# Kernel optimization log

Hardware: AMD Instinct MI355X
Metric: run time of the kernel (lower is better)

Reference implementation:

```python
import jax, jax.numpy as jnp
import numpy as np

# NOTE: the original torch code writes `torch.tensor(10 ^ -18)` which is Python
# bitwise XOR, i.e. the constant -28 (NOT 1e-18). We replicate that exact math.
RULE_OFFSET = -28.0


def setup_inputs() -> dict:
    key = jax.random.key(0)
    k0, k1, k2, k3 = jax.random.split(key, 4)
    batch, n_rules, n_fea = 8192, 256, 128
    data = jax.random.normal(k0, (batch, n_fea), dtype=jnp.float32)
    para_mu = jax.random.uniform(k1, (n_rules, n_fea), dtype=jnp.float32)
    para_sigma = jax.random.uniform(k2, (n_rules, n_fea), dtype=jnp.float32)
    para_w3 = jax.random.uniform(k3, (n_rules, n_fea + 1), dtype=jnp.float32)
    return {"data": data, "para_mu": para_mu, "para_sigma": para_sigma, "para_w3": para_w3}


def reference(data, para_mu, para_sigma, para_w3):
    # Gaussian fuzzification exponents: (batch, n_rules, n_fea)
    diff = data[:, None, :] - para_mu[None, :, :]
    exponent = -(diff ** 2) / (2.0 * para_sigma ** 2)
    # prod over features of exp(.) == exp(sum over features) -- same math, fused.
    layer_rule = jnp.exp(jnp.sum(exponent, axis=2))  # (batch, n_rules)
    layer_rule = layer_rule + RULE_OFFSET
    inv_frn = 1.0 / jnp.sum(layer_rule, axis=1, keepdims=True)  # (batch, 1)
    layer_normalize = layer_rule * inv_frn  # (batch, n_rules)
    # TSK consequent: w3[:,0] + sum_f w3[:,1:] * x
    layer_conq = para_w3[:, 0][None, :] + jnp.einsum('bf,rf->br', data, para_w3[:, 1:])
    layer_out_tsk = jnp.sum(layer_normalize * layer_conq, axis=1)  # (batch,)
    return jax.nn.sigmoid(layer_out_tsk)
```

## Files before the change

### kernel.cpp

```cpp
#include <hip/hip_runtime.h>
#include <math.h>

#define NR 256
#define NF 128
#define BCOLS 32

typedef short  s16x8  __attribute__((ext_vector_type(8)));
typedef __bf16 bf16x8 __attribute__((ext_vector_type(8)));
typedef float  f32x16 __attribute__((ext_vector_type(16)));

__device__ __forceinline__ unsigned short f2bf(float x) {
    unsigned int u = __float_as_uint(x);
    unsigned int r = (u + 0x7FFFu + ((u >> 16) & 1u)) >> 16;
    return (unsigned short)r;
}
__device__ __forceinline__ float bf2f(unsigned short b) {
    return __uint_as_float(((unsigned int)b) << 16);
}
__device__ __forceinline__ bf16x8 as_bf(s16x8 v) {
    return __builtin_bit_cast(bf16x8, v);
}
__device__ __forceinline__ f32x16 mfma_bf16(s16x8 a, s16x8 b, f32x16 acc) {
    return __builtin_amdgcn_mfma_f32_32x32x16_bf16(as_bf(a), as_bf(b), acc, 0, 0, 0);
}

__global__ __launch_bounds__(256) void prep2_kernel(
    const float* __restrict__ mu, const float* __restrict__ sigma,
    const float* __restrict__ w3,
    unsigned short* __restrict__ PH, unsigned short* __restrict__ PL,
    unsigned short* __restrict__ WC,
    float* __restrict__ Cr, float* __restrict__ W0)
{
    const int blk = blockIdx.x;
    if (blk < 32) {
        const int t    = blk * 256 + threadIdx.x;
        const int e    = t >> 6;
        const int lane = t & 63;
        const int rt   = e >> 4;
        const int ks2  = e & 15;
        const bool second = (ks2 >= 8);
        const int fb   = (ks2 & 7) * 16 + (lane >> 5) * 8;
        const int rule = rt * 32 + (lane & 31);

        const float* mrow = mu    + (size_t)rule * NF + fb;
        const float* srow = sigma + (size_t)rule * NF + fb;
        const float* wrow = w3    + (size_t)rule * (NF + 1) + 1 + fb;

        s16x8 vh, vl, vw;
        #pragma unroll
        for (int j = 0; j < 8; ++j) {
            const float s  = srow[j];
            const float m  = mrow[j];
            const float w  = wrow[j];
            const float u2 = -0.5f / fmaxf(s * s, 1e-30f);
            const float val = second ? (-2.0f * u2 * m) : u2;
            const unsigned short hh = f2bf(val);
            vh[j] = (short)hh;
            vl[j] = (short)f2bf(val - bf2f(hh));
            const unsigned short wh = f2bf(w);
            vw[j] = (short)(second ? f2bf(w - bf2f(wh)) : wh);
        }
        ((s16x8*)PH)[t] = vh;
        ((s16x8*)PL)[t] = vl;
        ((s16x8*)WC)[t] = vw;
    } else {
        const int rg   = blk - 32;
        const int rl   = threadIdx.x >> 3;
        const int jj   = threadIdx.x & 7;
        const int rule = rg * 32 + rl;
        const float* mrow = mu    + (size_t)rule * NF + jj * 16;
        const float* srow = sigma + (size_t)rule * NF + jj * 16;
        float cc = 0.f;
        #pragma unroll
        for (int q = 0; q < 16; q += 4) {
            const float4 s4 = *(const float4*)(srow + q);
            const float4 m4 = *(const float4*)(mrow + q);
            cc += (-0.5f / fmaxf(s4.x * s4.x, 1e-30f)) * m4.x * m4.x;
            cc += (-0.5f / fmaxf(s4.y * s4.y, 1e-30f)) * m4.y * m4.y;
            cc += (-0.5f / fmaxf(s4.z * s4.z, 1e-30f)) * m4.z * m4.z;
            cc += (-0.5f / fmaxf(s4.w * s4.w, 1e-30f)) * m4.w * m4.w;
        }
        cc += __shfl_down(cc, 4);
        cc += __shfl_down(cc, 2);
        cc += __shfl_down(cc, 1);
        if (jj == 0) {
            Cr[rule] = cc;
            W0[rule] = w3[(size_t)rule * (NF + 1)];
        }
    }
}

__global__ __launch_bounds__(512) void fnn_mfma(
    const float* __restrict__ data,
    const unsigned short* __restrict__ PH, const unsigned short* __restrict__ PL,
    const unsigned short* __restrict__ WC,
    const float* __restrict__ Cr, const float* __restrict__ W0,
    float* __restrict__ out)
{
    __shared__ s16x8 sBH[16][64], sBL[16][64];
    __shared__ float sCr[NR], sW0[NR];
    __shared__ float redD[8][BCOLS], redN[8][BCOLS];

    const int tid = threadIdx.x;
    if (tid < NR) sCr[tid] = Cr[tid];
    else          sW0[tid - NR] = W0[tid - NR];

    const int b0 = blockIdx.x * BCOLS;

    {
        const int bks = tid >> 6;
        const int bln = tid & 63;
        const float* p = data + (size_t)(b0 + (bln & 31)) * NF
                              + bks * 16 + (bln >> 5) * 8;
        const float4 v0 = *(const float4*)(p);
        const float4 v1 = *(const float4*)(p + 4);
        const float dv[8] = {v0.x, v0.y, v0.z, v0.w, v1.x, v1.y, v1.z, v1.w};
        s16x8 e_d, e_dl, e_d2, e_d2l;
        #pragma unroll
        for (int j = 0; j < 8; ++j) {
            const float d  = dv[j];
            const float d2 = d * d;
            const unsigned short dh  = f2bf(d);
            const unsigned short d2h = f2bf(d2);
            e_d  [j] = (short)dh;
            e_dl [j] = (short)f2bf(d  - bf2f(dh));
            e_d2 [j] = (short)d2h;
            e_d2l[j] = (short)f2bf(d2 - bf2f(d2h));
        }
        sBH[bks    ][bln] = e_d2;
        sBL[bks    ][bln] = e_d2l;
        sBH[bks + 8][bln] = e_d;
        sBL[bks + 8][bln] = e_dl;
    }
    __syncthreads();

    const int wv   = tid >> 6;
    const int lane = tid & 63;
    const int col  = lane & 31;
    const int half = lane >> 5;

    const s16x8* PHp = (const s16x8*)PH + (size_t)wv * 16 * 64 + lane;
    const s16x8* PLp = (const s16x8*)PL + (size_t)wv * 16 * 64 + lane;
    const s16x8* WCp = (const s16x8*)WC + (size_t)wv * 16 * 64 + lane;

    f32x16 accS0, accS1, accQ;
    #pragma unroll
    for (int e = 0; e < 16; ++e) { accS0[e] = 0.f; accS1[e] = 0.f; accQ[e] = 0.f; }

    s16x8 a0 = PHp[0], a1 = PLp[0], a2 = WCp[0];
    #pragma unroll 1
    for (int ks = 0; ks < 16; ++ks) {
        const int nofs = ((ks < 15) ? (ks + 1) : ks) * 64;
        const s16x8 n0 = PHp[nofs];
        const s16x8 n1 = PLp[nofs];
        const s16x8 n2 = WCp[nofs];

        const s16x8 bh = sBH[ks][lane];
        const s16x8 bl = sBL[ks][lane];
        accS0 = mfma_bf16(a0, bh, accS0);
        accS1 = mfma_bf16(a1, bh, accS1);
        accS1 = mfma_bf16(a0, bl, accS1);
        if (ks < 8) {
            accQ = mfma_bf16(a2, sBH[ks + 8][lane], accQ);
            accQ = mfma_bf16(a2, sBL[ks + 8][lane], accQ);
        } else {
            accQ = mfma_bf16(a2, bh, accQ);
        }
        a0 = n0; a1 = n1; a2 = n2;
    }

    float den_p = 0.f, num_p = 0.f;
    #pragma unroll
    for (int reg = 0; reg < 16; ++reg) {
        const int rloc = (reg & 3) + 8 * (reg >> 2) + 4 * half;
        const int rule = wv * 32 + rloc;
        const float S  = accS0[reg] + accS1[reg] + sCr[rule];
        const float rv = __expf(fminf(S, 0.f)) - 28.0f;
        const float cq = accQ[reg] + sW0[rule];
        den_p += rv;
        num_p += rv * cq;
    }
    den_p += __shfl_xor(den_p, 32);
    num_p += __shfl_xor(num_p, 32);
    if (half == 0) { redD[wv][col] = den_p; redN[wv][col] = num_p; }
    __syncthreads();

    if (tid < BCOLS) {
        float den = 0.f, num = 0.f;
        #pragma unroll
        for (int w = 0; w < 8; ++w) { den += redD[w][tid]; num += redN[w][tid]; }
        out[b0 + tid] = 1.0f / (1.0f + __expf(-(num / den)));
    }
}

#define TBF 8
__global__ __launch_bounds__(256) void fnn_fused(
    const float* __restrict__ data,
    const float* __restrict__ mu, const float* __restrict__ sigma,
    const float* __restrict__ w3,
    float* __restrict__ out)
{
    __shared__ float d_tile[TBF][NF];
    __shared__ float red[TBF][2][4];

    const int tid = threadIdx.x;
    const int b0  = blockIdx.x * TBF;
    {
        const float4* src = (const float4*)(data + (size_t)b0 * NF);
        ((float4*)(&d_tile[0][0]))[tid] = src[tid];
    }
    __syncthreads();

    const float* mu_r = mu    + (size_t)tid * NF;
    const float* sg_r = sigma + (size_t)tid * NF;
    const float* w_r  = w3    + (size_t)tid * (NF + 1);

    float S[TBF], Q[TBF];
    #pragma unroll
    for (int b = 0; b < TBF; ++b) { S[b] = 0.f; Q[b] = 0.f; }

    #pragma unroll 2
    for (int f = 0; f < NF; f += 4) {
        const float4 m4 = *(const float4*)(mu_r + f);
        const float4 s4 = *(const float4*)(sg_r + f);
        const float w0 = w_r[1 + f + 0], w1 = w_r[1 + f + 1];
        const float w2 = w_r[1 + f + 2], w3v = w_r[1 + f + 3];
        float4 c4;
        c4.x = -0.5f / fmaxf(s4.x * s4.x, 1e-30f);
        c4.y = -0.5f / fmaxf(s4.y * s4.y, 1e-30f);
        c4.z = -0.5f / fmaxf(s4.z * s4.z, 1e-30f);
        c4.w = -0.5f / fmaxf(s4.w * s4.w, 1e-30f);
        #pragma unroll
        for (int b = 0; b < TBF; ++b) {
            const float4 d4 = *(const float4*)(&d_tile[b][f]);
            float t;
            t = d4.x - m4.x; S[b] = fmaf(t * t, c4.x, S[b]); Q[b] = fmaf(d4.x, w0,  Q[b]);
            t = d4.y - m4.y; S[b] = fmaf(t * t, c4.y, S[b]); Q[b] = fmaf(d4.y, w1,  Q[b]);
            t = d4.z - m4.z; S[b] = fmaf(t * t, c4.z, S[b]); Q[b] = fmaf(d4.z, w2,  Q[b]);
            t = d4.w - m4.w; S[b] = fmaf(t * t, c4.w, S[b]); Q[b] = fmaf(d4.w, w3v, Q[b]);
        }
    }

    const float bias = w_r[0];
    #pragma unroll
    for (int b = 0; b < TBF; ++b) {
        float rule = __expf(S[b]) - 28.0f;
        float rc   = rule * (bias + Q[b]);
        #pragma unroll
        for (int off = 32; off > 0; off >>= 1) {
            rule += __shfl_down(rule, off);
            rc   += __shfl_down(rc,   off);
        }
        if ((tid & 63) == 0) {
            red[b][0][tid >> 6] = rule;
            red[b][1][tid >> 6] = rc;
        }
    }
    __syncthreads();
    if (tid < TBF) {
        const float den = red[tid][0][0] + red[tid][0][1] + red[tid][0][2] + red[tid][0][3];
        const float num = red[tid][1][0] + red[tid][1][1] + red[tid][1][2] + red[tid][1][3];
        out[b0 + tid] = 1.0f / (1.0f + __expf(-(num / den)));
    }
}

extern "C" void kernel_launch(void* const* d_in, const int* in_sizes, int n_in,
                              void* d_out, int out_size, void* d_ws, size_t ws_size,
                              hipStream_t stream) {
    const float* data  = (const float*)d_in[0];
    const float* mu    = (const float*)d_in[1];
    const float* sigma = (const float*)d_in[2];
    const float* w3    = (const float*)d_in[3];
    float* out = (float*)d_out;

    const int batch = in_sizes[0] / NF;
    const size_t need = 3u * 65536u * sizeof(unsigned short) + 2u * NR * sizeof(float);

    if (ws_size >= need && (batch % BCOLS) == 0) {
        unsigned short* PH = (unsigned short*)d_ws;
        unsigned short* PL = PH + 65536;
        unsigned short* WC = PL + 65536;
        float* Cr = (float*)(WC + 65536);
        float* W0 = Cr + NR;
        prep2_kernel<<<40, 256, 0, stream>>>(mu, sigma, w3, PH, PL, WC, Cr, W0);
        fnn_mfma<<<batch / BCOLS, 512, 0, stream>>>(data, PH, PL, WC, Cr, W0, out);
    } else {
        fnn_fused<<<batch / TBF, 256, 0, stream>>>(data, mu, sigma, w3, out);
    }
}
```

Baseline: 18.26 us.

## Fuse parameter prep into main MFMA kernel and drop low-part corrections

Removes the separate prep kernel and workspace buffers. Each block now recomputes the per-rule constants and the bf16 A operands from mu, sigma and w3 on the fly. The lo-part MFMA corrections for the quadratic term are dropped, going from three accumulators to one and cutting MFMA count. This saves a kernel launch but repeats the parameter transform and division in every block (256 blocks), and the lower bf16 precision in the exponent sum risks accuracy.

Result: slower. 33.56 us (+83.7%).

```diff
diff --git a/kernel.cpp b/kernel.cpp
--- a/kernel.cpp
+++ b/kernel.cpp
@@ -3,7 +3,6 @@
 
 #define NR 256
 #define NF 128
-#define BCOLS 32
 
 typedef short  s16x8  __attribute__((ext_vector_type(8)));
 typedef __bf16 bf16x8 __attribute__((ext_vector_type(8)));
@@ -24,88 +23,18 @@
     return __builtin_amdgcn_mfma_f32_32x32x16_bf16(as_bf(a), as_bf(b), acc, 0, 0, 0);
 }
 
-__global__ __launch_bounds__(256) void prep2_kernel(
+__global__ __launch_bounds__(512) void fnn_one(
+    const float* __restrict__ data,
     const float* __restrict__ mu, const float* __restrict__ sigma,
     const float* __restrict__ w3,
-    unsigned short* __restrict__ PH, unsigned short* __restrict__ PL,
-    unsigned short* __restrict__ WC,
-    float* __restrict__ Cr, float* __restrict__ W0)
-{
-    const int blk = blockIdx.x;
-    if (blk < 32) {
-        const int t    = blk * 256 + threadIdx.x;
-        const int e    = t >> 6;
-        const int lane = t & 63;
-        const int rt   = e >> 4;
-        const int ks2  = e & 15;
-        const bool second = (ks2 >= 8);
-        const int fb   = (ks2 & 7) * 16 + (lane >> 5) * 8;
-        const int rule = rt * 32 + (lane & 31);
-
-        const float* mrow = mu    + (size_t)rule * NF + fb;
-        const float* srow = sigma + (size_t)rule * NF + fb;
-        const float* wrow = w3    + (size_t)rule * (NF + 1) + 1 + fb;
-
-        s16x8 vh, vl, vw;
-        #pragma unroll
-        for (int j = 0; j < 8; ++j) {
-            const float s  = srow[j];
-            const float m  = mrow[j];
-            const float w  = wrow[j];
-            const float u2 = -0.5f / fmaxf(s * s, 1e-30f);
-            const float val = second ? (-2.0f * u2 * m) : u2;
-            const unsigned short hh = f2bf(val);
-            vh[j] = (short)hh;
-            vl[j] = (short)f2bf(val - bf2f(hh));
-            const unsigned short wh = f2bf(w);
-            vw[j] = (short)(second ? f2bf(w - bf2f(wh)) : wh);
-        }
-        ((s16x8*)PH)[t] = vh;
-        ((s16x8*)PL)[t] = vl;
-        ((s16x8*)WC)[t] = vw;
-    } else {
-        const int rg   = blk - 32;
-        const int rl   = threadIdx.x >> 3;
-        const int jj   = threadIdx.x & 7;
-        const int rule = rg * 32 + rl;
-        const float* mrow = mu    + (size_t)rule * NF + jj * 16;
-        const float* srow = sigma + (size_t)rule * NF + jj * 16;
-        float cc = 0.f;
-        #pragma unroll
-        for (int q = 0; q < 16; q += 4) {
-            const float4 s4 = *(const float4*)(srow + q);
-            const float4 m4 = *(const float4*)(mrow + q);
-            cc += (-0.5f / fmaxf(s4.x * s4.x, 1e-30f)) * m4.x * m4.x;
-            cc += (-0.5f / fmaxf(s4.y * s4.y, 1e-30f)) * m4.y * m4.y;
-            cc += (-0.5f / fmaxf(s4.z * s4.z, 1e-30f)) * m4.z * m4.z;
-            cc += (-0.5f / fmaxf(s4.w * s4.w, 1e-30f)) * m4.w * m4.w;
-        }
-        cc += __shfl_down(cc, 4);
-        cc += __shfl_down(cc, 2);
-        cc += __shfl_down(cc, 1);
-        if (jj == 0) {
-            Cr[rule] = cc;
-            W0[rule] = w3[(size_t)rule * (NF + 1)];
-        }
-    }
-}
-
-__global__ __launch_bounds__(512) void fnn_mfma(
-    const float* __restrict__ data,
-    const unsigned short* __restrict__ PH, const unsigned short* __restrict__ PL,
-    const unsigned short* __restrict__ WC,
-    const float* __restrict__ Cr, const float* __restrict__ W0,
     float* __restrict__ out)
 {
     __shared__ s16x8 sBH[16][64], sBL[16][64];
     __shared__ float sCr[NR], sW0[NR];
-    __shared__ float redD[8][BCOLS], redN[8][BCOLS];
+    __shared__ float redD[8][32], redN[8][32];
 
     const int tid = threadIdx.x;
-    if (tid < NR) sCr[tid] = Cr[tid];
-    else          sW0[tid - NR] = W0[tid - NR];
-
-    const int b0 = blockIdx.x * BCOLS;
+    const int b0  = blockIdx.x * 32;
 
     {
         const int bks = tid >> 6;
@@ -132,6 +61,26 @@
         sBH[bks + 8][bln] = e_d;
         sBL[bks + 8][bln] = e_dl;
     }
+
+    {
+        const int r   = tid >> 1;
+        const int seg = tid & 1;
+        const float* mrow = mu    + (size_t)r * NF + seg * 64;
+        const float* srow = sigma + (size_t)r * NF + seg * 64;
+        float cc = 0.f;
+        #pragma unroll 4
+        for (int q = 0; q < 64; q += 4) {
+            const float4 s4 = *(const float4*)(srow + q);
+            const float4 m4 = *(const float4*)(mrow + q);
+            cc += (-0.5f / fmaxf(s4.x * s4.x, 1e-30f)) * m4.x * m4.x;
+            cc += (-0.5f / fmaxf(s4.y * s4.y, 1e-30f)) * m4.y * m4.y;
+            cc += (-0.5f / fmaxf(s4.z * s4.z, 1e-30f)) * m4.z * m4.z;
+            cc += (-0.5f / fmaxf(s4.w * s4.w, 1e-30f)) * m4.w * m4.w;
+        }
+        cc += __shfl_xor(cc, 1);
+        if (seg == 0) sCr[r] = cc;
+        if (tid < NR) sW0[tid] = w3[(size_t)tid * (NF + 1)];
+    }
     __syncthreads();
 
     const int wv   = tid >> 6;
@@ -139,34 +88,56 @@
     const int col  = lane & 31;
     const int half = lane >> 5;
 
-    const s16x8* PHp = (const s16x8*)PH + (size_t)wv * 16 * 64 + lane;
-    const s16x8* PLp = (const s16x8*)PL + (size_t)wv * 16 * 64 + lane;
-    const s16x8* WCp = (const s16x8*)WC + (size_t)wv * 16 * 64 + lane;
-
-    f32x16 accS0, accS1, accQ;
-    #pragma unroll
-    for (int e = 0; e < 16; ++e) { accS0[e] = 0.f; accS1[e] = 0.f; accQ[e] = 0.f; }
-
-    s16x8 a0 = PHp[0], a1 = PLp[0], a2 = WCp[0];
+    const int r  = wv * 32 + (lane & 31);
+    const int fh = half * 8;
+    const float* mrow = mu    + (size_t)r * NF;
+    const float* srow = sigma + (size_t)r * NF;
+    const float* wrow = w3    + (size_t)r * (NF + 1) + 1;
+
+    f32x16 accS, accQ;
+    #pragma unroll
+    for (int e = 0; e < 16; ++e) { accS[e] = 0.f; accQ[e] = 0.f; }
+
     #pragma unroll 1
     for (int ks = 0; ks < 16; ++ks) {
-        const int nofs = ((ks < 15) ? (ks + 1) : ks) * 64;
-        const s16x8 n0 = PHp[nofs];
-        const s16x8 n1 = PLp[nofs];
-        const s16x8 n2 = WCp[nofs];
+        const int f0 = (ks & 7) * 16 + fh;
+        const float4 m40 = *(const float4*)(mrow + f0);
+        const float4 m41 = *(const float4*)(mrow + f0 + 4);
+        const float4 s40 = *(const float4*)(srow + f0);
+        const float4 s41 = *(const float4*)(srow + f0 + 4);
+        const float mv[8] = {m40.x, m40.y, m40.z, m40.w, m41.x, m41.y, m41.z, m41.w};
+        const float sv[8] = {s40.x, s40.y, s40.z, s40.w, s41.x, s41.y, s41.z, s41.w};
+
+        s16x8 a0, a2;
+        if (ks < 8) {
+            #pragma unroll
+            for (int j = 0; j < 8; ++j) {
+                const float s  = sv[j];
+                const float u2 = -0.5f / fmaxf(s * s, 1e-30f);
+                a0[j] = (short)f2bf(u2);
+                a2[j] = (short)f2bf(wrow[f0 + j]);
+            }
+        } else {
+            #pragma unroll
+            for (int j = 0; j < 8; ++j) {
+                const float s  = sv[j];
+                const float m  = mv[j];
+                const float u2 = -0.5f / fmaxf(s * s, 1e-30f);
+                a0[j] = (short)f2bf(-2.0f * u2 * m);
+                const float w  = wrow[f0 + j];
+                const unsigned short wh = f2bf(w);
+                a2[j] = (short)f2bf(w - bf2f(wh));
+            }
+        }
 
         const s16x8 bh = sBH[ks][lane];
-        const s16x8 bl = sBL[ks][lane];
-        accS0 = mfma_bf16(a0, bh, accS0);
-        accS1 = mfma_bf16(a1, bh, accS1);
-        accS1 = mfma_bf16(a0, bl, accS1);
+        accS = mfma_bf16(a0, bh, accS);
         if (ks < 8) {
             accQ = mfma_bf16(a2, sBH[ks + 8][lane], accQ);
             accQ = mfma_bf16(a2, sBL[ks + 8][lane], accQ);
         } else {
             accQ = mfma_bf16(a2, bh, accQ);
         }
-        a0 = n0; a1 = n1; a2 = n2;
     }
 
     float den_p = 0.f, num_p = 0.f;
@@ -174,7 +145,7 @@
     for (int reg = 0; reg < 16; ++reg) {
         const int rloc = (reg & 3) + 8 * (reg >> 2) + 4 * half;
         const int rule = wv * 32 + rloc;
-        const float S  = accS0[reg] + accS1[reg] + sCr[rule];
+        const float S  = accS[reg] + sCr[rule];
         const float rv = __expf(fminf(S, 0.f)) - 28.0f;
         const float cq = accQ[reg] + sW0[rule];
         den_p += rv;
@@ -185,7 +156,7 @@
     if (half == 0) { redD[wv][col] = den_p; redN[wv][col] = num_p; }
     __syncthreads();
 
-    if (tid < BCOLS) {
+    if (tid < 32) {
         float den = 0.f, num = 0.f;
         #pragma unroll
         for (int w = 0; w < 8; ++w) { den += redD[w][tid]; num += redN[w][tid]; }
@@ -274,16 +245,9 @@
     float* out = (float*)d_out;
 
     const int batch = in_sizes[0] / NF;
-    const size_t need = 3u * 65536u * sizeof(unsigned short) + 2u * NR * sizeof(float);
-
-    if (ws_size >= need && (batch % BCOLS) == 0) {
-        unsigned short* PH = (unsigned short*)d_ws;
-        unsigned short* PL = PH + 65536;
-        unsigned short* WC = PL + 65536;
-        float* Cr = (float*)(WC + 65536);
-        float* W0 = Cr + NR;
-        prep2_kernel<<<40, 256, 0, stream>>>(mu, sigma, w3, PH, PL, WC, Cr, W0);
-        fnn_mfma<<<batch / BCOLS, 512, 0, stream>>>(data, PH, PL, WC, Cr, W0, out);
+
+    if ((batch % 32) == 0) {
+        fnn_one<<<batch / 32, 512, 0, stream>>>(data, mu, sigma, w3, out);
     } else {
         fnn_fused<<<batch / TBF, 256, 0, stream>>>(data, mu, sigma, w3, out);
     }
```

## Drop low-order bf16 split for Gaussian exponent and fully unroll MFMA loop

Applied to the files above, without the earlier changes.

Removes the PL low-part array and the error-compensation MFMAs for the exponent sum, keeping a single bf16 term for the exponent and d^2 while retaining the split only for the consequent weights. This cuts the MFMA count per k-step and one global stream of A-operand loads. The k-loop is fully unrolled with double-buffered register prefetch and sched barriers to overlap global loads with MFMA work. The risk is lower accuracy in the exponent sum, which is then amplified by exp.

Result: faster. 15.95 us (-12.6%).

```diff
diff --git a/kernel.cpp b/kernel.cpp
--- a/kernel.cpp
+++ b/kernel.cpp
@@ -3,7 +3,6 @@
 
 #define NR 256
 #define NF 128
-#define BCOLS 32
 
 typedef short  s16x8  __attribute__((ext_vector_type(8)));
 typedef __bf16 bf16x8 __attribute__((ext_vector_type(8)));
@@ -24,11 +23,10 @@
     return __builtin_amdgcn_mfma_f32_32x32x16_bf16(as_bf(a), as_bf(b), acc, 0, 0, 0);
 }
 
-__global__ __launch_bounds__(256) void prep2_kernel(
+__global__ __launch_bounds__(256) void prep2s_kernel(
     const float* __restrict__ mu, const float* __restrict__ sigma,
     const float* __restrict__ w3,
-    unsigned short* __restrict__ PH, unsigned short* __restrict__ PL,
-    unsigned short* __restrict__ WC,
+    unsigned short* __restrict__ PH, unsigned short* __restrict__ WC,
     float* __restrict__ Cr, float* __restrict__ W0)
 {
     const int blk = blockIdx.x;
@@ -46,7 +44,7 @@
         const float* srow = sigma + (size_t)rule * NF + fb;
         const float* wrow = w3    + (size_t)rule * (NF + 1) + 1 + fb;
 
-        s16x8 vh, vl, vw;
+        s16x8 vh, vw;
         #pragma unroll
         for (int j = 0; j < 8; ++j) {
             const float s  = srow[j];
@@ -54,14 +52,11 @@
             const float w  = wrow[j];
             const float u2 = -0.5f / fmaxf(s * s, 1e-30f);
             const float val = second ? (-2.0f * u2 * m) : u2;
-            const unsigned short hh = f2bf(val);
-            vh[j] = (short)hh;
-            vl[j] = (short)f2bf(val - bf2f(hh));
+            vh[j] = (short)f2bf(val);
             const unsigned short wh = f2bf(w);
             vw[j] = (short)(second ? f2bf(w - bf2f(wh)) : wh);
         }
         ((s16x8*)PH)[t] = vh;
-        ((s16x8*)PL)[t] = vl;
         ((s16x8*)WC)[t] = vw;
     } else {
         const int rg   = blk - 32;
@@ -92,20 +87,19 @@
 
 __global__ __launch_bounds__(512) void fnn_mfma(
     const float* __restrict__ data,
-    const unsigned short* __restrict__ PH, const unsigned short* __restrict__ PL,
-    const unsigned short* __restrict__ WC,
+    const unsigned short* __restrict__ PH, const unsigned short* __restrict__ WC,
     const float* __restrict__ Cr, const float* __restrict__ W0,
     float* __restrict__ out)
 {
-    __shared__ s16x8 sBH[16][64], sBL[16][64];
+    __shared__ s16x8 sB0[8][64], sB1[8][64], sB2[8][64];
     __shared__ float sCr[NR], sW0[NR];
-    __shared__ float redD[8][BCOLS], redN[8][BCOLS];
+    __shared__ float redD[8][32], redN[8][32];
 
     const int tid = threadIdx.x;
     if (tid < NR) sCr[tid] = Cr[tid];
     else          sW0[tid - NR] = W0[tid - NR];
 
-    const int b0 = blockIdx.x * BCOLS;
+    const int b0 = blockIdx.x * 32;
 
     {
         const int bks = tid >> 6;
@@ -115,22 +109,18 @@
         const float4 v0 = *(const float4*)(p);
         const float4 v1 = *(const float4*)(p + 4);
         const float dv[8] = {v0.x, v0.y, v0.z, v0.w, v1.x, v1.y, v1.z, v1.w};
-        s16x8 e_d, e_dl, e_d2, e_d2l;
+        s16x8 e_d2, e_d, e_dl;
         #pragma unroll
         for (int j = 0; j < 8; ++j) {
             const float d  = dv[j];
-            const float d2 = d * d;
-            const unsigned short dh  = f2bf(d);
-            const unsigned short d2h = f2bf(d2);
-            e_d  [j] = (short)dh;
-            e_dl [j] = (short)f2bf(d  - bf2f(dh));
-            e_d2 [j] = (short)d2h;
-            e_d2l[j] = (short)f2bf(d2 - bf2f(d2h));
-        }
-        sBH[bks    ][bln] = e_d2;
-        sBL[bks    ][bln] = e_d2l;
-        sBH[bks + 8][bln] = e_d;
-        sBL[bks + 8][bln] = e_dl;
+            const unsigned short dh = f2bf(d);
+            e_d2[j] = (short)f2bf(d * d);
+            e_d [j] = (short)dh;
+            e_dl[j] = (short)f2bf(d - bf2f(dh));
+        }
+        sB0[bks][bln] = e_d2;
+        sB1[bks][bln] = e_d;
+        sB2[bks][bln] = e_dl;
     }
     __syncthreads();
 
@@ -140,41 +130,77 @@
     const int half = lane >> 5;
 
     const s16x8* PHp = (const s16x8*)PH + (size_t)wv * 16 * 64 + lane;
-    const s16x8* PLp = (const s16x8*)PL + (size_t)wv * 16 * 64 + lane;
     const s16x8* WCp = (const s16x8*)WC + (size_t)wv * 16 * 64 + lane;
 
-    f32x16 accS0, accS1, accQ;
+    f32x16 accS, accQ;
     #pragma unroll
-    for (int e = 0; e < 16; ++e) { accS0[e] = 0.f; accS1[e] = 0.f; accQ[e] = 0.f; }
-
-    s16x8 a0 = PHp[0], a1 = PLp[0], a2 = WCp[0];
-    #pragma unroll 1
-    for (int ks = 0; ks < 16; ++ks) {
-        const int nofs = ((ks < 15) ? (ks + 1) : ks) * 64;
-        const s16x8 n0 = PHp[nofs];
-        const s16x8 n1 = PLp[nofs];
-        const s16x8 n2 = WCp[nofs];
-
-        const s16x8 bh = sBH[ks][lane];
-        const s16x8 bl = sBL[ks][lane];
-        accS0 = mfma_bf16(a0, bh, accS0);
-        accS1 = mfma_bf16(a1, bh, accS1);
-        accS1 = mfma_bf16(a0, bl, accS1);
-        if (ks < 8) {
-            accQ = mfma_bf16(a2, sBH[ks + 8][lane], accQ);
-            accQ = mfma_bf16(a2, sBL[ks + 8][lane], accQ);
-        } else {
-            accQ = mfma_bf16(a2, bh, accQ);
-        }
-        a0 = n0; a1 = n1; a2 = n2;
-    }
+    for (int e = 0; e < 16; ++e) { accS[e] = 0.f; accQ[e] = 0.f; }
+
+    s16x8 X0h, X0w, X1h, X1w, X2h, X2w, X3h, X3w;
+    s16x8 Y0h, Y0w, Y1h, Y1w, Y2h, Y2w, Y3h, Y3w;
+
+#define LOADX(G) \
+    X0h = PHp[((G)*4+0)*64]; X0w = WCp[((G)*4+0)*64]; \
+    X1h = PHp[((G)*4+1)*64]; X1w = WCp[((G)*4+1)*64]; \
+    X2h = PHp[((G)*4+2)*64]; X2w = WCp[((G)*4+2)*64]; \
+    X3h = PHp[((G)*4+3)*64]; X3w = WCp[((G)*4+3)*64];
+#define LOADY(G) \
+    Y0h = PHp[((G)*4+0)*64]; Y0w = WCp[((G)*4+0)*64]; \
+    Y1h = PHp[((G)*4+1)*64]; Y1w = WCp[((G)*4+1)*64]; \
+    Y2h = PHp[((G)*4+2)*64]; Y2w = WCp[((G)*4+2)*64]; \
+    Y3h = PHp[((G)*4+3)*64]; Y3w = WCp[((G)*4+3)*64];
+
+#define KS_LO(AH, AW, KM)                            \
+    {                                                 \
+        const s16x8 b2 = sB0[KM][lane];               \
+        const s16x8 bh = sB1[KM][lane];               \
+        const s16x8 bl = sB2[KM][lane];               \
+        accS = mfma_bf16(AH, b2, accS);               \
+        accQ = mfma_bf16(AW, bh, accQ);               \
+        accQ = mfma_bf16(AW, bl, accQ);               \
+    }
+#define KS_HI(AH, AW, KM)                            \
+    {                                                 \
+        const s16x8 bh = sB1[KM][lane];               \
+        accS = mfma_bf16(AH, bh, accS);               \
+        accQ = mfma_bf16(AW, bh, accQ);               \
+    }
+
+    LOADX(0)
+    LOADY(1)
+    KS_LO(X0h, X0w, 0)
+    KS_LO(X1h, X1w, 1)
+    KS_LO(X2h, X2w, 2)
+    KS_LO(X3h, X3w, 3)
+    __builtin_amdgcn_sched_barrier(0);
+    LOADX(2)
+    KS_LO(Y0h, Y0w, 4)
+    KS_LO(Y1h, Y1w, 5)
+    KS_LO(Y2h, Y2w, 6)
+    KS_LO(Y3h, Y3w, 7)
+    __builtin_amdgcn_sched_barrier(0);
+    LOADY(3)
+    KS_HI(X0h, X0w, 0)
+    KS_HI(X1h, X1w, 1)
+    KS_HI(X2h, X2w, 2)
+    KS_HI(X3h, X3w, 3)
+    __builtin_amdgcn_sched_barrier(0);
+    KS_HI(Y0h, Y0w, 4)
+    KS_HI(Y1h, Y1w, 5)
+    KS_HI(Y2h, Y2w, 6)
+    KS_HI(Y3h, Y3w, 7)
+
+#undef LOADX
+#undef LOADY
+#undef KS_LO
+#undef KS_HI
 
     float den_p = 0.f, num_p = 0.f;
     #pragma unroll
     for (int reg = 0; reg < 16; ++reg) {
         const int rloc = (reg & 3) + 8 * (reg >> 2) + 4 * half;
         const int rule = wv * 32 + rloc;
-        const float S  = accS0[reg] + accS1[reg] + sCr[rule];
+        const float S  = accS[reg] + sCr[rule];
         const float rv = __expf(fminf(S, 0.f)) - 28.0f;
         const float cq = accQ[reg] + sW0[rule];
         den_p += rv;
@@ -185,7 +211,7 @@
     if (half == 0) { redD[wv][col] = den_p; redN[wv][col] = num_p; }
     __syncthreads();
 
-    if (tid < BCOLS) {
+    if (tid < 32) {
         float den = 0.f, num = 0.f;
         #pragma unroll
         for (int w = 0; w < 8; ++w) { den += redD[w][tid]; num += redN[w][tid]; }
@@ -274,16 +300,15 @@
     float* out = (float*)d_out;
 
     const int batch = in_sizes[0] / NF;
-    const size_t need = 3u * 65536u * sizeof(unsigned short) + 2u * NR * sizeof(float);
-
-    if (ws_size >= need && (batch % BCOLS) == 0) {
+    const size_t need = 2u * 65536u * sizeof(unsigned short) + 2u * NR * sizeof(float);
+
+    if (ws_size >= need && (batch % 32) == 0) {
         unsigned short* PH = (unsigned short*)d_ws;
-        unsigned short* PL = PH + 65536;
-        unsigned short* WC = PL + 65536;
+        unsigned short* WC = PH + 65536;
         float* Cr = (float*)(WC + 65536);
         float* W0 = Cr + NR;
-        prep2_kernel<<<40, 256, 0, stream>>>(mu, sigma, w3, PH, PL, WC, Cr, W0);
-        fnn_mfma<<<batch / BCOLS, 512, 0, stream>>>(data, PH, PL, WC, Cr, W0, out);
+        prep2s_kernel<<<40, 256, 0, stream>>>(mu, sigma, w3, PH, WC, Cr, W0);
+        fnn_mfma<<<batch / 32, 512, 0, stream>>>(data, PH, WC, Cr, W0, out);
     } else {
         fnn_fused<<<batch / TBF, 256, 0, stream>>>(data, mu, sigma, w3, out);
     }
```
